# Kernel optimization log

Hardware: AMD Instinct MI355X
Metric: run time of the kernel (lower is better)

Reference implementation:

```python
import jax, jax.numpy as jnp
from jax import lax
import numpy as np

N_CENTER, N_NEAR, COUT = 1024, 32, 256


def fps(xyz, m):
    # farthest point sampling -> [B, m] int32 indices
    B, N, _ = xyz.shape
    dist0 = jnp.full((B, N), 1e10, xyz.dtype)
    far0 = jnp.zeros((B,), jnp.int32)

    def step(carry, _):
        dists, far = carry
        cen = jax.vmap(lambda p, i: p[i])(xyz, far)            # [B,3]
        d = jnp.sum((xyz - cen[:, None, :]) ** 2, axis=-1)     # [B,N]
        dists = jnp.minimum(dists, d)
        nxt = jnp.argmax(dists, axis=-1).astype(jnp.int32)
        return (dists, nxt), far

    _, idx = lax.scan(step, (dist0, far0), None, length=m)
    return jnp.transpose(idx)                                   # [B,m]


def knn(xyz, k):
    # euclidean kNN over all points -> [B,N,k] (stand-in for surface_knn)
    sq = jnp.sum(xyz ** 2, axis=-1)                             # [B,N]
    d = sq[:, :, None] + sq[:, None, :] - 2.0 * jnp.einsum('bnd,bmd->bnm', xyz, xyz)
    _, idx = lax.top_k(-d, k)
    return idx


def gather(x, idx):
    # index_points: x [B,N,...], idx [B,S] or [B,S,K]
    return jax.vmap(lambda p, i: p[i])(x, idx)


def point_attention(center_fea, group_fea, wq, wk, wv):
    # center_fea [B,S,Cin], group_fea [B,S,K,D] -> [B,S,COUT]
    q = jnp.einsum('bsc,ch->bsh', center_fea, wq)
    k = jnp.einsum('bskd,dh->bskh', group_fea, wk)
    v = jnp.einsum('bskd,dh->bskh', group_fea, wv)
    scores = jnp.einsum('bsh,bskh->bsk', q, k) / jnp.sqrt(jnp.asarray(COUT, q.dtype))
    attn = jax.nn.softmax(scores, axis=-1)
    return jnp.einsum('bsk,bskh->bsh', attn, v)


def _forward(xyz, mad, adj, pt, mad_fea, adj_fea, pt_fea, cst_fea,
             wq_mad, wk_mad, wv_mad, wq_adj, wk_adj, wv_adj,
             wq_pt, wk_pt, wv_pt, wq_cst, wk_cst, wv_cst):
    idx_all = knn(xyz, N_NEAR)                  # [B,N,K]
    fps_idx = fps(xyz, N_CENTER)                # [B,S]

    center_xyz = gather(xyz, fps_idx)
    center_mad = gather(mad, fps_idx)
    center_adj = gather(adj, fps_idx)
    center_pt = gather(pt, fps_idx)
    c_mad_fea = gather(mad_fea, fps_idx)
    c_adj_fea = gather(adj_fea, fps_idx)
    c_pt_fea = gather(pt_fea, fps_idx)
    c_cst_fea = gather(cst_fea, fps_idx)

    idx = gather(idx_all, fps_idx)              # [B,S,K]
    g_xyz = gather(xyz, idx)
    g_mad = gather(mad, idx)
    g_adj = gather(adj, idx)
    g_pt = gather(pt, idx)
    g_mad_fea = gather(mad_fea, idx)
    g_adj_fea = gather(adj_fea, idx)
    g_pt_fea = gather(pt_fea, idx)
    g_cst_fea = gather(cst_fea, idx)

    mad_rel = g_mad - center_mad[:, :, None, :]
    adj_cat = jnp.concatenate([g_adj, jnp.broadcast_to(center_adj[:, :, None, :], g_adj.shape)], axis=-1)
    pt_cat = jnp.concatenate([g_pt, jnp.broadcast_to(center_pt[:, :, None, :], g_pt.shape)], axis=-1)
    xyz_rel = g_xyz - center_xyz[:, :, None, :]

    g_mad_fea = jnp.concatenate([g_mad_fea, mad_rel], axis=-1)
    g_adj_fea = jnp.concatenate([g_adj_fea, adj_cat], axis=-1)
    g_pt_fea = jnp.concatenate([g_pt_fea, pt_cat], axis=-1)
    g_cst_fea = jnp.concatenate([g_cst_fea, xyz_rel], axis=-1)

    o_mad = point_attention(c_mad_fea, g_mad_fea, wq_mad, wk_mad, wv_mad)
    o_adj = point_attention(c_adj_fea, g_adj_fea, wq_adj, wk_adj, wv_adj)
    o_pt = point_attention(c_pt_fea, g_pt_fea, wq_pt, wk_pt, wv_pt)
    o_cst = point_attention(c_cst_fea, g_cst_fea, wq_cst, wk_cst, wv_cst)

    return (center_xyz, center_mad, center_adj, center_pt, o_mad, o_adj, o_pt, o_cst)


def setup_inputs() -> dict:
    key = jax.random.key(0)
    ks = jax.random.split(key, 24)
    B, N, C = 4, 4096, 128
    inp = {
        'xyz': jax.random.normal(ks[0], (B, N, 3), jnp.float32),
        'mad': jax.random.normal(ks[1], (B, N, 3), jnp.float32),
        'adj': jax.random.uniform(ks[2], (B, N, 2), jnp.float32),
        'pt': jax.random.uniform(ks[3], (B, N, 4), jnp.float32),
        'mad_fea': jax.random.normal(ks[4], (B, N, C), jnp.float32),
        'adj_fea': jax.random.normal(ks[5], (B, N, C), jnp.float32),
        'pt_fea': jax.random.normal(ks[6], (B, N, C), jnp.float32),
        'cst_fea': jax.random.normal(ks[7], (B, N, C), jnp.float32),
    }
    dims = {'wq_mad': C, 'wk_mad': C + 3, 'wv_mad': C + 3,
            'wq_adj': C, 'wk_adj': C + 4, 'wv_adj': C + 4,
            'wq_pt': C, 'wk_pt': C + 8, 'wv_pt': C + 8,
            'wq_cst': C, 'wk_cst': C + 3, 'wv_cst': C + 3}
    for i, (name, d) in enumerate(dims.items()):
        inp[name] = jax.random.normal(ks[8 + i], (d, COUT), jnp.float32) * 0.02
    return inp


def reference(xyz, mad, adj, pt, mad_fea, adj_fea, pt_fea, cst_fea,
              wq_mad, wk_mad, wv_mad, wq_adj, wk_adj, wv_adj,
              wq_pt, wk_pt, wv_pt, wq_cst, wk_cst, wv_cst):
    return _forward(xyz, mad, adj, pt, mad_fea, adj_fea, pt_fea, cst_fea,
                    wq_mad, wk_mad, wv_mad, wq_adj, wk_adj, wv_adj,
                    wq_pt, wk_pt, wv_pt, wq_cst, wk_cst, wv_cst)
```

## Files before the change

### kernel.cpp

```cpp
#include <hip/hip_runtime.h>

#define BATCH 4
#define NPTS  4096
#define NC    1024
#define KNN   32
#define CIN   128
#define CO    256
#define DP    136

#define OFF_CXYZ 0
#define OFF_CMAD (BATCH*NC*3)
#define OFF_CADJ (OFF_CMAD + BATCH*NC*3)
#define OFF_CPT  (OFF_CADJ + BATCH*NC*2)
#define OFF_OMAD (OFF_CPT  + BATCH*NC*4)
#define OFF_OADJ (OFF_OMAD + BATCH*NC*CO)
#define OFF_OPT  (OFF_OADJ + BATCH*NC*CO)
#define OFF_OCST (OFF_OPT  + BATCH*NC*CO)

typedef unsigned long long u64;

template<bool MAXI>
__device__ __forceinline__ u64 wave_red_u64(u64 k)
{
    const int oldv = MAXI ? 0 : -1;
#define DPP_STEP(C)                                                              \
    {                                                                            \
        unsigned plo = (unsigned)__builtin_amdgcn_update_dpp(oldv, (int)(unsigned)k,        C, 0xf, 0xf, false); \
        unsigned phi = (unsigned)__builtin_amdgcn_update_dpp(oldv, (int)(unsigned)(k>>32),  C, 0xf, 0xf, false); \
        u64 p = ((u64)phi << 32) | plo;                                          \
        if (MAXI ? (p > k) : (p < k)) k = p;                                     \
    }
    DPP_STEP(0x111) DPP_STEP(0x112) DPP_STEP(0x114)
    DPP_STEP(0x118) DPP_STEP(0x142) DPP_STEP(0x143)
#undef DPP_STEP
    return k;
}

__global__ __launch_bounds__(512) void fps_prep_kernel(
    const float* __restrict__ xyz, int* __restrict__ fps_idx,
    const float* __restrict__ wq_mad, const float* __restrict__ wk_mad, const float* __restrict__ wv_mad,
    const float* __restrict__ wq_adj, const float* __restrict__ wk_adj, const float* __restrict__ wv_adj,
    const float* __restrict__ wq_pt,  const float* __restrict__ wk_pt,  const float* __restrict__ wv_pt,
    const float* __restrict__ wq_cst, const float* __restrict__ wk_cst, const float* __restrict__ wv_cst,
    float* __restrict__ M, float* __restrict__ Wvp)
{
    __shared__ float4 s_xyz[NPTS];
    __shared__ u64    s_ck[2][8];
    const int t = threadIdx.x;

    if (blockIdx.x >= BATCH) {
        const int r    = blockIdx.x - BATCH;
        const int type = r / DP;
        const int row  = r - type * DP;
        const float* wq; const float* wk; const float* wv; int D;
        if (type == 0)      { wq=wq_mad; wk=wk_mad; wv=wv_mad; D=131; }
        else if (type == 1) { wq=wq_adj; wk=wk_adj; wv=wv_adj; D=132; }
        else if (type == 2) { wq=wq_pt;  wk=wk_pt;  wv=wv_pt;  D=136; }
        else                { wq=wq_cst; wk=wk_cst; wv=wv_cst; D=131; }

        if (t < CO)
            Wvp[((size_t)type*DP + row)*CO + t] = (row < D) ? wv[(size_t)row*CO + t] : 0.f;

        if (row < CIN) {
            float* sq = (float*)s_xyz;
            if (t < CO) sq[t] = wq[(size_t)row*CO + t];
            __syncthreads();
            if (t < DP) {
                float acc = 0.f;
                if (t < D) {
                    const float* wkr = wk + (size_t)t * CO;
                    for (int h = 0; h < CO; h += 4) {
                        float4 a = *(const float4*)&wkr[h];
                        float4 b4 = *(const float4*)&sq[h];
                        acc = fmaf(a.x,b4.x,acc); acc = fmaf(a.y,b4.y,acc);
                        acc = fmaf(a.z,b4.z,acc); acc = fmaf(a.w,b4.w,acc);
                    }
                }
                M[((size_t)type*CIN + row)*DP + t] = acc;
            }
        }
        return;
    }

    const int b = blockIdx.x;
    const float* xb = xyz + (size_t)b * NPTS * 3;

    float px[8], py[8], pz[8], dd[8];
    unsigned inv[8];
#pragma unroll
    for (int i = 0; i < 8; ++i) {
        int p = t + i * 512;
        px[i] = xb[p*3+0]; py[i] = xb[p*3+1]; pz[i] = xb[p*3+2];
        s_xyz[p] = make_float4(px[i], py[i], pz[i], 0.f);
        dd[i] = 1e10f;
        inv[i] = ~(unsigned)p;
    }
    __syncthreads();

    int far = 0;
    float cx = xb[0], cy = xb[1], cz = xb[2];
    for (int s = 0; s < NC; ++s) {
        if (t == 0) fps_idx[b*NC + s] = far;
        u64 K[8];
#pragma unroll
        for (int i = 0; i < 8; ++i) {
            float dx = __fsub_rn(px[i], cx);
            float dy = __fsub_rn(py[i], cy);
            float dz = __fsub_rn(pz[i], cz);
            float d  = __fadd_rn(__fadd_rn(__fmul_rn(dx,dx), __fmul_rn(dy,dy)), __fmul_rn(dz,dz));
            float nd = fminf(dd[i], d);
            dd[i] = nd;
            K[i] = ((u64)__float_as_uint(nd) << 32) | inv[i];
        }
#pragma unroll
        for (int st = 4; st >= 1; st >>= 1)
#pragma unroll
            for (int j = 0; j < st; ++j)
                if (K[j+st] > K[j]) K[j] = K[j+st];
        u64 k = wave_red_u64<true>(K[0]);

        const int buf = s & 1;
        if ((t & 63) == 63) s_ck[buf][t>>6] = k;
        __syncthreads();
        u64 c0 = s_ck[buf][0], c1 = s_ck[buf][1], c2 = s_ck[buf][2], c3 = s_ck[buf][3];
        u64 c4 = s_ck[buf][4], c5 = s_ck[buf][5], c6 = s_ck[buf][6], c7 = s_ck[buf][7];
        if (c1 > c0) c0 = c1;  if (c3 > c2) c2 = c3;
        if (c5 > c4) c4 = c5;  if (c7 > c6) c6 = c7;
        if (c2 > c0) c0 = c2;  if (c6 > c4) c4 = c6;
        if (c4 > c0) c0 = c4;
        far = (int)~((unsigned)c0);
        float4 c = s_xyz[far];
        cx = c.x; cy = c.y; cz = c.z;
    }
}

template<int TYPE>
__device__ __forceinline__ void attn_t(
    int b, int bs0, int ci,
    const float* __restrict__ fea, const float* __restrict__ aux,
    const float* __restrict__ Mt, const float* __restrict__ Wvpt,
    float* __restrict__ outp,
    float (*s_cf)[CIN], float (*s_u)[DP], float (*s_fea)[KNN][DP],
    float (*s_sc)[KNN], float (*s_wf)[DP], const int (*s_nbr4)[KNN])
{
    const int t = threadIdx.x, g = t >> 6, l = t & 63;
    const int l31 = l & 31, h32 = l >> 5;

    if (l < 32) {
        float4 v = *(const float4*)&fea[((size_t)(b*NPTS + ci))*CIN + l*4];
        *(float4*)&s_cf[g][l*4] = v;
    }
#pragma unroll
    for (int it = 0; it < 16; ++it) {
        int kk = it*2 + h32;
        int j  = s_nbr4[g][kk];
        float4 v = *(const float4*)&fea[((size_t)(b*NPTS + j))*CIN + l31*4];
        *(float4*)&s_fea[g][kk][l31*4] = v;
    }
    if (l < KNN) {
        int j = s_nbr4[g][l];
        float pad[8];
        if (TYPE == 0 || TYPE == 3) {
#pragma unroll
            for (int i = 0; i < 3; ++i)
                pad[i] = aux[(size_t)(b*NPTS + j)*3 + i] - aux[(size_t)(b*NPTS + ci)*3 + i];
            pad[3]=pad[4]=pad[5]=pad[6]=pad[7]=0.f;
        } else if (TYPE == 1) {
            pad[0] = aux[(size_t)(b*NPTS + j)*2 + 0];
            pad[1] = aux[(size_t)(b*NPTS + j)*2 + 1];
            pad[2] = aux[(size_t)(b*NPTS + ci)*2 + 0];
            pad[3] = aux[(size_t)(b*NPTS + ci)*2 + 1];
            pad[4]=pad[5]=pad[6]=pad[7]=0.f;
        } else {
#pragma unroll
            for (int i = 0; i < 4; ++i) pad[i]   = aux[(size_t)(b*NPTS + j)*4 + i];
#pragma unroll
            for (int i = 0; i < 4; ++i) pad[4+i] = aux[(size_t)(b*NPTS + ci)*4 + i];
        }
#pragma unroll
        for (int i = 0; i < 8; ++i) s_fea[g][l][CIN+i] = pad[i];
    }
    __syncthreads();

#pragma unroll
    for (int j = 0; j < 3; ++j) {
        int d = l + 64*j;
        if (d < DP) {
            float acc = 0.f;
            for (int c = 0; c < CIN; c += 4) {
                float4 cf4 = *(const float4*)&s_cf[g][c];
                acc = fmaf(cf4.x, Mt[(size_t)(c+0)*DP + d], acc);
                acc = fmaf(cf4.y, Mt[(size_t)(c+1)*DP + d], acc);
                acc = fmaf(cf4.z, Mt[(size_t)(c+2)*DP + d], acc);
                acc = fmaf(cf4.w, Mt[(size_t)(c+3)*DP + d], acc);
            }
            s_u[g][d] = acc;
        }
    }
    __syncthreads();

#pragma unroll
    for (int it = 0; it < 16; ++it) {
        int kk = it*2 + h32;
        float acc = 0.f;
        for (int c = l31; c < DP/4; c += 32) {
            float4 f4 = *(const float4*)&s_fea[g][kk][c*4];
            float4 u4 = *(const float4*)&s_u[g][c*4];
            acc = fmaf(f4.x,u4.x,acc); acc = fmaf(f4.y,u4.y,acc);
            acc = fmaf(f4.z,u4.z,acc); acc = fmaf(f4.w,u4.w,acc);
        }
#pragma unroll
        for (int off = 16; off; off >>= 1) acc += __shfl_xor(acc, off);
        if (l31 == 0) s_sc[g][kk] = acc * 0.0625f;
    }
    __syncthreads();

    if (l < KNN) {
        float sc = s_sc[g][l];
        float m = sc;
#pragma unroll
        for (int off = 16; off; off >>= 1) m = fmaxf(m, __shfl_xor(m, off));
        float e = expf(sc - m);
        float ssum = e;
#pragma unroll
        for (int off = 16; off; off >>= 1) ssum += __shfl_xor(ssum, off);
        s_sc[g][l] = e / ssum;
    }
    __syncthreads();

    if (l < DP/4) {
        const int d0 = l*4;
        float w0=0.f, w1=0.f, w2=0.f, w3=0.f;
#pragma unroll
        for (int k4 = 0; k4 < KNN; k4 += 4) {
            float4 a  = *(const float4*)&s_sc[g][k4];
            float4 f0 = *(const float4*)&s_fea[g][k4+0][d0];
            float4 f1 = *(const float4*)&s_fea[g][k4+1][d0];
            float4 f2 = *(const float4*)&s_fea[g][k4+2][d0];
            float4 f3 = *(const float4*)&s_fea[g][k4+3][d0];
            w0=fmaf(a.x,f0.x,w0); w1=fmaf(a.x,f0.y,w1); w2=fmaf(a.x,f0.z,w2); w3=fmaf(a.x,f0.w,w3);
            w0=fmaf(a.y,f1.x,w0); w1=fmaf(a.y,f1.y,w1); w2=fmaf(a.y,f1.z,w2); w3=fmaf(a.y,f1.w,w3);
            w0=fmaf(a.z,f2.x,w0); w1=fmaf(a.z,f2.y,w1); w2=fmaf(a.z,f2.z,w2); w3=fmaf(a.z,f2.w,w3);
            w0=fmaf(a.w,f3.x,w0); w1=fmaf(a.w,f3.y,w1); w2=fmaf(a.w,f3.z,w2); w3=fmaf(a.w,f3.w,w3);
        }
        s_wf[g][d0+0]=w0; s_wf[g][d0+1]=w1; s_wf[g][d0+2]=w2; s_wf[g][d0+3]=w3;
    }
    __syncthreads();

    float o0=0.f, o1=0.f, o2=0.f, o3=0.f;
    for (int d4 = 0; d4 < DP/4; ++d4) {
        float4 wf0 = *(const float4*)&s_wf[0][d4*4];
        float4 wf1 = *(const float4*)&s_wf[1][d4*4];
        float4 wf2 = *(const float4*)&s_wf[2][d4*4];
        float4 wf3 = *(const float4*)&s_wf[3][d4*4];
        float v0 = Wvpt[(size_t)(d4*4+0)*CO + t];
        float v1 = Wvpt[(size_t)(d4*4+1)*CO + t];
        float v2 = Wvpt[(size_t)(d4*4+2)*CO + t];
        float v3 = Wvpt[(size_t)(d4*4+3)*CO + t];
        o0=fmaf(wf0.x,v0,o0); o0=fmaf(wf0.y,v1,o0); o0=fmaf(wf0.z,v2,o0); o0=fmaf(wf0.w,v3,o0);
        o1=fmaf(wf1.x,v0,o1); o1=fmaf(wf1.y,v1,o1); o1=fmaf(wf1.z,v2,o1); o1=fmaf(wf1.w,v3,o1);
        o2=fmaf(wf2.x,v0,o2); o2=fmaf(wf2.y,v1,o2); o2=fmaf(wf2.z,v2,o2); o2=fmaf(wf2.w,v3,o2);
        o3=fmaf(wf3.x,v0,o3); o3=fmaf(wf3.y,v1,o3); o3=fmaf(wf3.z,v2,o3); o3=fmaf(wf3.w,v3,o3);
    }
    outp[(size_t)(bs0+0)*CO + t] = o0;
    outp[(size_t)(bs0+1)*CO + t] = o1;
    outp[(size_t)(bs0+2)*CO + t] = o2;
    outp[(size_t)(bs0+3)*CO + t] = o3;
    __syncthreads();
}

__global__ __launch_bounds__(256, 2) void attn_kernel(
    const float* __restrict__ xyz, const float* __restrict__ mad,
    const float* __restrict__ adj, const float* __restrict__ pt,
    const float* __restrict__ mad_fea, const float* __restrict__ adj_fea,
    const float* __restrict__ pt_fea,  const float* __restrict__ cst_fea,
    const float* __restrict__ M, const float* __restrict__ Wvp,
    const int* __restrict__ fps_idx,
    float* __restrict__ out)
{
    __shared__ float s_cf[4][CIN];
    __shared__ float s_u[4][DP];
    __shared__ float s_fea[4][KNN][DP];
    __shared__ float s_sc[4][KNN];
    __shared__ float s_wf[4][DP];
    __shared__ int   s_nbr4[4][KNN];

    const int bs0 = blockIdx.x * 4;
    const int b   = bs0 >> 10;
    const int t   = threadIdx.x;
    const int g   = t >> 6, l = t & 63;
    const float* xb = xyz + (size_t)b * NPTS * 3;

    const int ci = fps_idx[bs0 + g];

    if (l < 3)             out[OFF_CXYZ + (bs0+g)*3 + l]      = xb[(size_t)ci*3 + l];
    if (l >= 4 && l < 7)   out[OFF_CMAD + (bs0+g)*3 + (l-4)]  = mad[(size_t)(b*NPTS+ci)*3 + (l-4)];
    if (l >= 8 && l < 10)  out[OFF_CADJ + (bs0+g)*2 + (l-8)]  = adj[(size_t)(b*NPTS+ci)*2 + (l-8)];
    if (l >= 12 && l < 16) out[OFF_CPT  + (bs0+g)*4 + (l-12)] = pt[(size_t)(b*NPTS+ci)*4 + (l-12)];

    {
        const float cx = xb[ci*3], cy = xb[ci*3+1], cz = xb[ci*3+2];
        const float sqc = __fadd_rn(__fadd_rn(__fmul_rn(cx,cx), __fmul_rn(cy,cy)), __fmul_rn(cz,cz));

        unsigned du[64];
#pragma unroll
        for (int j = 0; j < 64; ++j) {
            int p = l + (j << 6);
            float x = xb[p*3], y = xb[p*3+1], z = xb[p*3+2];
            float sqm = __fadd_rn(__fadd_rn(__fmul_rn(x,x), __fmul_rn(y,y)), __fmul_rn(z,z));
            float dot = __fadd_rn(__fadd_rn(__fmul_rn(cx,x), __fmul_rn(cy,y)), __fmul_rn(cz,z));
            float dv  = __fsub_rn(__fadd_rn(sqc, sqm), __fmul_rn(2.0f, dot));
            unsigned u = __float_as_uint(dv);
            u ^= (unsigned)(((int)u >> 31)) | 0x80000000u;
            du[j] = u;
        }
        u64 gk[4];
#pragma unroll
        for (int G2 = 0; G2 < 4; ++G2) {
            int j0 = G2*16;
            u64 m = ((u64)du[j0] << 32) | (unsigned)(l + (j0 << 6));
#pragma unroll
            for (int jj = 1; jj < 16; ++jj) {
                int j = j0 + jj;
                u64 kj = ((u64)du[j] << 32) | (unsigned)(l + (j << 6));
                if (kj < m) m = kj;
            }
            gk[G2] = m;
        }

        for (int kk = 0; kk < KNN; ++kk) {
            u64 m01 = gk[0] < gk[1] ? gk[0] : gk[1];
            u64 m23 = gk[2] < gk[3] ? gk[2] : gk[3];
            u64 kmin = m01 < m23 ? m01 : m23;
            u64 kw = wave_red_u64<false>(kmin);
            int widx = __shfl((int)(unsigned)kw, 63);
            if (l == 0) s_nbr4[g][kk] = widx;
            int wj = widx >> 6;
            if ((widx & 63) == l) {
#pragma unroll
                for (int G2 = 0; G2 < 4; ++G2) {
                    if ((wj >> 4) == G2) {
#pragma unroll
                        for (int jj = 0; jj < 16; ++jj)
                            if (wj == G2*16 + jj) du[G2*16 + jj] = 0xFFFFFFFFu;
                        int j0 = G2*16;
                        u64 m = ((u64)du[j0] << 32) | (unsigned)(l + (j0 << 6));
#pragma unroll
                        for (int jj = 1; jj < 16; ++jj) {
                            int j = j0 + jj;
                            u64 kj = ((u64)du[j] << 32) | (unsigned)(l + (j << 6));
                            if (kj < m) m = kj;
                        }
                        gk[G2] = m;
                    }
                }
            }
        }
    }

    attn_t<0>(b, bs0, ci, mad_fea, mad, M + 0*CIN*DP, Wvp + 0*DP*CO, out + OFF_OMAD,
              s_cf, s_u, s_fea, s_sc, s_wf, s_nbr4);
    attn_t<1>(b, bs0, ci, adj_fea, adj, M + 1*CIN*DP, Wvp + 1*DP*CO, out + OFF_OADJ,
              s_cf, s_u, s_fea, s_sc, s_wf, s_nbr4);
    attn_t<2>(b, bs0, ci, pt_fea,  pt,  M + 2*CIN*DP, Wvp + 2*DP*CO, out + OFF_OPT,
              s_cf, s_u, s_fea, s_sc, s_wf, s_nbr4);
    attn_t<3>(b, bs0, ci, cst_fea, xyz, M + 3*CIN*DP, Wvp + 3*DP*CO, out + OFF_OCST,
              s_cf, s_u, s_fea, s_sc, s_wf, s_nbr4);
}

extern "C" void kernel_launch(void* const* d_in, const int* in_sizes, int n_in,
                              void* d_out, int out_size, void* d_ws, size_t ws_size,
                              hipStream_t stream)
{
    const float* xyz     = (const float*)d_in[0];
    const float* mad     = (const float*)d_in[1];
    const float* adj     = (const float*)d_in[2];
    const float* pt      = (const float*)d_in[3];
    const float* mad_fea = (const float*)d_in[4];
    const float* adj_fea = (const float*)d_in[5];
    const float* pt_fea  = (const float*)d_in[6];
    const float* cst_fea = (const float*)d_in[7];
    const float* wq_mad  = (const float*)d_in[8];
    const float* wk_mad  = (const float*)d_in[9];
    const float* wv_mad  = (const float*)d_in[10];
    const float* wq_adj  = (const float*)d_in[11];
    const float* wk_adj  = (const float*)d_in[12];
    const float* wv_adj  = (const float*)d_in[13];
    const float* wq_pt   = (const float*)d_in[14];
    const float* wk_pt   = (const float*)d_in[15];
    const float* wv_pt   = (const float*)d_in[16];
    const float* wq_cst  = (const float*)d_in[17];
    const float* wk_cst  = (const float*)d_in[18];
    const float* wv_cst  = (const float*)d_in[19];
    float* out = (float*)d_out;

    int*   fps_idx = (int*)d_ws;
    float* M       = (float*)(fps_idx + BATCH*NC);
    float* Wvp     = M + 4*CIN*DP;

    fps_prep_kernel<<<BATCH + 4*DP, 512, 0, stream>>>(xyz, fps_idx,
        wq_mad, wk_mad, wv_mad, wq_adj, wk_adj, wv_adj,
        wq_pt, wk_pt, wv_pt, wq_cst, wk_cst, wv_cst, M, Wvp);
    attn_kernel<<<BATCH*NC/4, 256, 0, stream>>>(xyz, mad, adj, pt,
        mad_fea, adj_fea, pt_fea, cst_fea, M, Wvp, fps_idx, out);
}
```

Before: 1.176 ms.

## Split kNN into separate kernel and use 32-bit FPS wave reductions

The neighbour-selection loop moves out of the attention kernel into its own knn_kernel, which writes neighbour indices to workspace. The attention kernel only loads those indices, and its launch_bounds min-blocks hint is dropped because it no longer holds the 64-register distance array. The FPS loop now reduces a float max followed by a u32 index min instead of a 64-bit packed key, and buffers the sampled indices in shared memory so they are written to global once at the end. This adds an extra launch and a global round trip for the indices, and the two-step reduction adds a shuffle to the serial FPS critical path.

After: 1.169 ms. No clear change (-0.6%).

```diff
diff --git a/kernel.cpp b/kernel.cpp
--- a/kernel.cpp
+++ b/kernel.cpp
@@ -19,21 +19,46 @@
 
 typedef unsigned long long u64;
 
-template<bool MAXI>
-__device__ __forceinline__ u64 wave_red_u64(u64 k)
-{
-    const int oldv = MAXI ? 0 : -1;
+__device__ __forceinline__ u64 wave_min_u64(u64 k)
+{
 #define DPP_STEP(C)                                                              \
     {                                                                            \
-        unsigned plo = (unsigned)__builtin_amdgcn_update_dpp(oldv, (int)(unsigned)k,        C, 0xf, 0xf, false); \
-        unsigned phi = (unsigned)__builtin_amdgcn_update_dpp(oldv, (int)(unsigned)(k>>32),  C, 0xf, 0xf, false); \
+        unsigned plo = (unsigned)__builtin_amdgcn_update_dpp(-1, (int)(unsigned)k,        C, 0xf, 0xf, false); \
+        unsigned phi = (unsigned)__builtin_amdgcn_update_dpp(-1, (int)(unsigned)(k>>32),  C, 0xf, 0xf, false); \
         u64 p = ((u64)phi << 32) | plo;                                          \
-        if (MAXI ? (p > k) : (p < k)) k = p;                                     \
+        if (p < k) k = p;                                                        \
     }
     DPP_STEP(0x111) DPP_STEP(0x112) DPP_STEP(0x114)
     DPP_STEP(0x118) DPP_STEP(0x142) DPP_STEP(0x143)
 #undef DPP_STEP
     return k;
+}
+
+__device__ __forceinline__ float wave_max_f32(float v)
+{
+#define DPP_STEP(C)                                                              \
+    {                                                                            \
+        float p = __int_as_float(__builtin_amdgcn_update_dpp(                    \
+            __float_as_int(-1.0f), __float_as_int(v), C, 0xf, 0xf, false));      \
+        v = fmaxf(v, p);                                                         \
+    }
+    DPP_STEP(0x111) DPP_STEP(0x112) DPP_STEP(0x114)
+    DPP_STEP(0x118) DPP_STEP(0x142) DPP_STEP(0x143)
+#undef DPP_STEP
+    return v;
+}
+
+__device__ __forceinline__ unsigned wave_min_u32(unsigned x)
+{
+#define DPP_STEP(C)                                                              \
+    {                                                                            \
+        unsigned p = (unsigned)__builtin_amdgcn_update_dpp(-1, (int)x, C, 0xf, 0xf, false); \
+        x = (p < x) ? p : x;                                                     \
+    }
+    DPP_STEP(0x111) DPP_STEP(0x112) DPP_STEP(0x114)
+    DPP_STEP(0x118) DPP_STEP(0x142) DPP_STEP(0x143)
+#undef DPP_STEP
+    return x;
 }
 
 __global__ __launch_bounds__(512) void fps_prep_kernel(
@@ -46,6 +71,7 @@
 {
     __shared__ float4 s_xyz[NPTS];
     __shared__ u64    s_ck[2][8];
+    __shared__ int    s_far_out[NC];
     const int t = threadIdx.x;
 
     if (blockIdx.x >= BATCH) {
@@ -86,22 +112,20 @@
     const float* xb = xyz + (size_t)b * NPTS * 3;
 
     float px[8], py[8], pz[8], dd[8];
-    unsigned inv[8];
 #pragma unroll
     for (int i = 0; i < 8; ++i) {
         int p = t + i * 512;
         px[i] = xb[p*3+0]; py[i] = xb[p*3+1]; pz[i] = xb[p*3+2];
         s_xyz[p] = make_float4(px[i], py[i], pz[i], 0.f);
         dd[i] = 1e10f;
-        inv[i] = ~(unsigned)p;
     }
     __syncthreads();
 
     int far = 0;
     float cx = xb[0], cy = xb[1], cz = xb[2];
     for (int s = 0; s < NC; ++s) {
-        if (t == 0) fps_idx[b*NC + s] = far;
-        u64 K[8];
+        if (t == 0) s_far_out[s] = far;
+        float bv = -1.0f; unsigned bi = 0;
 #pragma unroll
         for (int i = 0; i < 8; ++i) {
             float dx = __fsub_rn(px[i], cx);
@@ -110,27 +134,101 @@
             float d  = __fadd_rn(__fadd_rn(__fmul_rn(dx,dx), __fmul_rn(dy,dy)), __fmul_rn(dz,dz));
             float nd = fminf(dd[i], d);
             dd[i] = nd;
-            K[i] = ((u64)__float_as_uint(nd) << 32) | inv[i];
-        }
-#pragma unroll
-        for (int st = 4; st >= 1; st >>= 1)
-#pragma unroll
-            for (int j = 0; j < st; ++j)
-                if (K[j+st] > K[j]) K[j] = K[j+st];
-        u64 k = wave_red_u64<true>(K[0]);
+            if (nd > bv) { bv = nd; bi = (unsigned)(t + i*512); }
+        }
+        float vw = wave_max_f32(bv);
+        float vstar = __shfl(vw, 63);
+        unsigned cand = (bv == vstar) ? bi : 0xFFFFFFFFu;
+        unsigned iw = wave_min_u32(cand);
 
         const int buf = s & 1;
-        if ((t & 63) == 63) s_ck[buf][t>>6] = k;
+        if ((t & 63) == 63)
+            s_ck[buf][t>>6] = ((u64)__float_as_uint(vstar) << 32) | (u64)(~iw);
         __syncthreads();
         u64 c0 = s_ck[buf][0], c1 = s_ck[buf][1], c2 = s_ck[buf][2], c3 = s_ck[buf][3];
         u64 c4 = s_ck[buf][4], c5 = s_ck[buf][5], c6 = s_ck[buf][6], c7 = s_ck[buf][7];
-        if (c1 > c0) c0 = c1;  if (c3 > c2) c2 = c3;
-        if (c5 > c4) c4 = c5;  if (c7 > c6) c6 = c7;
-        if (c2 > c0) c0 = c2;  if (c6 > c4) c4 = c6;
+        if (c1 > c0) c0 = c1;
+        if (c3 > c2) c2 = c3;
+        if (c5 > c4) c4 = c5;
+        if (c7 > c6) c6 = c7;
+        if (c2 > c0) c0 = c2;
+        if (c6 > c4) c4 = c6;
         if (c4 > c0) c0 = c4;
         far = (int)~((unsigned)c0);
         float4 c = s_xyz[far];
         cx = c.x; cy = c.y; cz = c.z;
+    }
+    __syncthreads();
+    for (int i = t; i < NC; i += 512) fps_idx[b*NC + i] = s_far_out[i];
+}
+
+__global__ __launch_bounds__(256) void knn_kernel(const float* __restrict__ xyz,
+                                                  const int* __restrict__ fps_idx,
+                                                  int* __restrict__ nbr_idx)
+{
+    const int bs0 = blockIdx.x * 4;
+    const int b   = bs0 >> 10;
+    const int t   = threadIdx.x;
+    const int g   = t >> 6, l = t & 63;
+    const float* xb = xyz + (size_t)b * NPTS * 3;
+
+    const int ci = fps_idx[bs0 + g];
+    const float cx = xb[ci*3], cy = xb[ci*3+1], cz = xb[ci*3+2];
+    const float sqc = __fadd_rn(__fadd_rn(__fmul_rn(cx,cx), __fmul_rn(cy,cy)), __fmul_rn(cz,cz));
+
+    unsigned du[64];
+#pragma unroll
+    for (int j = 0; j < 64; ++j) {
+        int p = l + (j << 6);
+        float x = xb[p*3], y = xb[p*3+1], z = xb[p*3+2];
+        float sqm = __fadd_rn(__fadd_rn(__fmul_rn(x,x), __fmul_rn(y,y)), __fmul_rn(z,z));
+        float dot = __fadd_rn(__fadd_rn(__fmul_rn(cx,x), __fmul_rn(cy,y)), __fmul_rn(cz,z));
+        float dv  = __fsub_rn(__fadd_rn(sqc, sqm), __fmul_rn(2.0f, dot));
+        unsigned u = __float_as_uint(dv);
+        u ^= (unsigned)(((int)u >> 31)) | 0x80000000u;
+        du[j] = u;
+    }
+    u64 gk[4];
+#pragma unroll
+    for (int G = 0; G < 4; ++G) {
+        int j0 = G*16;
+        u64 m = ((u64)du[j0] << 32) | (unsigned)(l + (j0 << 6));
+#pragma unroll
+        for (int jj = 1; jj < 16; ++jj) {
+            int j = j0 + jj;
+            u64 kj = ((u64)du[j] << 32) | (unsigned)(l + (j << 6));
+            if (kj < m) m = kj;
+        }
+        gk[G] = m;
+    }
+
+    int* nb = nbr_idx + (size_t)(bs0 + g) * KNN;
+    for (int kk = 0; kk < KNN; ++kk) {
+        u64 m01 = gk[0] < gk[1] ? gk[0] : gk[1];
+        u64 m23 = gk[2] < gk[3] ? gk[2] : gk[3];
+        u64 kw = wave_min_u64(m01 < m23 ? m01 : m23);
+        unsigned widx = (unsigned)__shfl((int)(unsigned)kw, 63);
+        if (l == 0) nb[kk] = (int)widx;
+        if ((widx & 63u) == (unsigned)l) {
+            int wj = (int)(widx >> 6);
+#pragma unroll
+            for (int G = 0; G < 4; ++G) {
+                if ((wj >> 4) == G) {
+#pragma unroll
+                    for (int jj = 0; jj < 16; ++jj)
+                        if (wj == G*16 + jj) du[G*16 + jj] = 0xFFFFFFFFu;
+                    int j0 = G*16;
+                    u64 m = ((u64)du[j0] << 32) | (unsigned)(l + (j0 << 6));
+#pragma unroll
+                    for (int jj = 1; jj < 16; ++jj) {
+                        int j = j0 + jj;
+                        u64 kj = ((u64)du[j] << 32) | (unsigned)(l + (j << 6));
+                        if (kj < m) m = kj;
+                    }
+                    gk[G] = m;
+                }
+            }
+        }
     }
 }
 
@@ -269,13 +367,13 @@
     __syncthreads();
 }
 
-__global__ __launch_bounds__(256, 2) void attn_kernel(
+__global__ __launch_bounds__(256) void attn_kernel(
     const float* __restrict__ xyz, const float* __restrict__ mad,
     const float* __restrict__ adj, const float* __restrict__ pt,
     const float* __restrict__ mad_fea, const float* __restrict__ adj_fea,
     const float* __restrict__ pt_fea,  const float* __restrict__ cst_fea,
     const float* __restrict__ M, const float* __restrict__ Wvp,
-    const int* __restrict__ fps_idx,
+    const int* __restrict__ fps_idx, const int* __restrict__ nbr_idx,
     float* __restrict__ out)
 {
     __shared__ float s_cf[4][CIN];
@@ -292,71 +390,13 @@
     const float* xb = xyz + (size_t)b * NPTS * 3;
 
     const int ci = fps_idx[bs0 + g];
+    if (t < 128) s_nbr4[t>>5][t&31] = nbr_idx[(size_t)(bs0 + (t>>5))*KNN + (t&31)];
 
     if (l < 3)             out[OFF_CXYZ + (bs0+g)*3 + l]      = xb[(size_t)ci*3 + l];
     if (l >= 4 && l < 7)   out[OFF_CMAD + (bs0+g)*3 + (l-4)]  = mad[(size_t)(b*NPTS+ci)*3 + (l-4)];
     if (l >= 8 && l < 10)  out[OFF_CADJ + (bs0+g)*2 + (l-8)]  = adj[(size_t)(b*NPTS+ci)*2 + (l-8)];
     if (l >= 12 && l < 16) out[OFF_CPT  + (bs0+g)*4 + (l-12)] = pt[(size_t)(b*NPTS+ci)*4 + (l-12)];
-
-    {
-        const float cx = xb[ci*3], cy = xb[ci*3+1], cz = xb[ci*3+2];
-        const float sqc = __fadd_rn(__fadd_rn(__fmul_rn(cx,cx), __fmul_rn(cy,cy)), __fmul_rn(cz,cz));
-
-        unsigned du[64];
-#pragma unroll
-        for (int j = 0; j < 64; ++j) {
-            int p = l + (j << 6);
-            float x = xb[p*3], y = xb[p*3+1], z = xb[p*3+2];
-            float sqm = __fadd_rn(__fadd_rn(__fmul_rn(x,x), __fmul_rn(y,y)), __fmul_rn(z,z));
-            float dot = __fadd_rn(__fadd_rn(__fmul_rn(cx,x), __fmul_rn(cy,y)), __fmul_rn(cz,z));
-            float dv  = __fsub_rn(__fadd_rn(sqc, sqm), __fmul_rn(2.0f, dot));
-            unsigned u = __float_as_uint(dv);
-            u ^= (unsigned)(((int)u >> 31)) | 0x80000000u;
-            du[j] = u;
-        }
-        u64 gk[4];
-#pragma unroll
-        for (int G2 = 0; G2 < 4; ++G2) {
-            int j0 = G2*16;
-            u64 m = ((u64)du[j0] << 32) | (unsigned)(l + (j0 << 6));
-#pragma unroll
-            for (int jj = 1; jj < 16; ++jj) {
-                int j = j0 + jj;
-                u64 kj = ((u64)du[j] << 32) | (unsigned)(l + (j << 6));
-                if (kj < m) m = kj;
-            }
-            gk[G2] = m;
-        }
-
-        for (int kk = 0; kk < KNN; ++kk) {
-            u64 m01 = gk[0] < gk[1] ? gk[0] : gk[1];
-            u64 m23 = gk[2] < gk[3] ? gk[2] : gk[3];
-            u64 kmin = m01 < m23 ? m01 : m23;
-            u64 kw = wave_red_u64<false>(kmin);
-            int widx = __shfl((int)(unsigned)kw, 63);
-            if (l == 0) s_nbr4[g][kk] = widx;
-            int wj = widx >> 6;
-            if ((widx & 63) == l) {
-#pragma unroll
-                for (int G2 = 0; G2 < 4; ++G2) {
-                    if ((wj >> 4) == G2) {
-#pragma unroll
-                        for (int jj = 0; jj < 16; ++jj)
-                            if (wj == G2*16 + jj) du[G2*16 + jj] = 0xFFFFFFFFu;
-                        int j0 = G2*16;
-                        u64 m = ((u64)du[j0] << 32) | (unsigned)(l + (j0 << 6));
-#pragma unroll
-                        for (int jj = 1; jj < 16; ++jj) {
-                            int j = j0 + jj;
-                            u64 kj = ((u64)du[j] << 32) | (unsigned)(l + (j << 6));
-                            if (kj < m) m = kj;
-                        }
-                        gk[G2] = m;
-                    }
-                }
-            }
-        }
-    }
+    __syncthreads();
 
     attn_t<0>(b, bs0, ci, mad_fea, mad, M + 0*CIN*DP, Wvp + 0*DP*CO, out + OFF_OMAD,
               s_cf, s_u, s_fea, s_sc, s_wf, s_nbr4);
@@ -395,12 +435,14 @@
     float* out = (float*)d_out;
 
     int*   fps_idx = (int*)d_ws;
-    float* M       = (float*)(fps_idx + BATCH*NC);
+    int*   nbr_idx = fps_idx + BATCH*NC;
+    float* M       = (float*)(nbr_idx + BATCH*NC*KNN);
     float* Wvp     = M + 4*CIN*DP;
 
     fps_prep_kernel<<<BATCH + 4*DP, 512, 0, stream>>>(xyz, fps_idx,
         wq_mad, wk_mad, wv_mad, wq_adj, wk_adj, wv_adj,
         wq_pt, wk_pt, wv_pt, wq_cst, wk_cst, wv_cst, M, Wvp);
+    knn_kernel<<<BATCH*NC/4, 256, 0, stream>>>(xyz, fps_idx, nbr_idx);
     attn_kernel<<<BATCH*NC/4, 256, 0, stream>>>(xyz, mad, adj, pt,
-        mad_fea, adj_fea, pt_fea, cst_fea, M, Wvp, fps_idx, out);
-}
+        mad_fea, adj_fea, pt_fea, cst_fea, M, Wvp, fps_idx, nbr_idx, out);
+}
```
